# Kernel optimization log

Measured on AMD Instinct MI355X. Metric: run time of the kernel, lower is better.

## Reference

```python
import jax, jax.numpy as jnp
import numpy as np
from jax import lax

DIM = 128
N_CODEBOOKS = 8
CODEBOOK_SIZE = 2048
BATCH = 16
TOKENS = 2048


def setup_inputs() -> dict:
    key = jax.random.key(0)
    k1, k2 = jax.random.split(key)
    x = jax.random.normal(k1, (BATCH, DIM, TOKENS), dtype=jnp.float32)
    # matches nn.Parameter(torch.randn(K, D) / D**0.5) per stage, stacked
    codebooks = jax.random.normal(k2, (N_CODEBOOKS, CODEBOOK_SIZE, DIM),
                                  dtype=jnp.float32) / jnp.sqrt(jnp.float32(DIM))
    return {"x": x, "codebooks": codebooks}


def reference(x, codebooks):
    """Residual VQ forward.

    x: (B, D, T), codebooks: (n_cb, K, D)
    Returns (total_quantized (B,D,T), codes (B,n_cb,T) int32, commitment_loss scalar)
    """
    xt = jnp.transpose(x, (0, 2, 1))  # (B, T, D)

    def step(carry, cb):
        residual, total = carry  # (B,T,D) each; cb: (K,D)
        # squared euclidean distances: ||r||^2 - 2 r.c + ||c||^2 -> (B,T,K)
        dist = (jnp.sum(residual * residual, axis=-1, keepdims=True)
                - 2.0 * jnp.einsum('btd,kd->btk', residual, cb)
                + jnp.sum(cb * cb, axis=-1))
        idx = jnp.argmin(dist, axis=-1)          # (B, T)
        quantized = cb[idx]                       # gather -> (B, T, D)
        # straight-through combine
        q_st = residual + lax.stop_gradient(quantized - residual)
        total = total + q_st
        residual = residual - lax.stop_gradient(quantized)
        # F.mse_loss(residual.detach(), zeros) == mean(residual**2), detached
        loss = jnp.mean(lax.stop_gradient(residual) ** 2)
        return (residual, total), (idx.astype(jnp.int32), loss)

    init = (xt, jnp.zeros_like(xt))
    (_, total), (codes, losses) = lax.scan(step, init, codebooks)
    total_quantized = jnp.transpose(total, (0, 2, 1))   # (B, D, T)
    codes = jnp.transpose(codes, (1, 0, 2))             # (B, n_cb, T)
    commitment_loss = jnp.sum(losses)
    return total_quantized, codes, commitment_loss
```

## Files before the change

### kernel.cpp

```cpp
#include <hip/hip_runtime.h>

#define DIM 128
#define NCB 8
#define KSZ 2048
#define BATCH 16
#define TOK 2048
#define NTOK (BATCH * TOK)
#define NELEM (BATCH * DIM * TOK)
#define T_TILE 128
#define NTHR 512
#define CHUNK 32
#define NCHUNK 16
#define GCODES 512

typedef float f32x4 __attribute__((ext_vector_type(4)));
typedef _Float16 f16x8 __attribute__((ext_vector_type(8)));

__global__ void rvq_prep_f16(const float* __restrict__ cbs,
                             _Float16* __restrict__ chf) {
    int i = blockIdx.x * 256 + threadIdx.x;
    chf[i] = (_Float16)cbs[i];
}

__global__ void rvq_cnorm(const float* __restrict__ cbs,
                          float* __restrict__ cnorm,
                          float* __restrict__ loss_acc) {
    if (blockIdx.x == 0 && threadIdx.x == 0) *loss_acc = 0.0f;
    int k = blockIdx.x * 256 + threadIdx.x;
    const float4* row = (const float4*)(cbs + (size_t)k * DIM);
    float s = 0.0f;
#pragma unroll
    for (int i = 0; i < DIM / 4; ++i) {
        float4 v = row[i];
        s += v.x * v.x + v.y * v.y + v.z * v.z + v.w * v.w;
    }
    cnorm[k] = s;
}

__global__ __launch_bounds__(NTHR, 2) void rvq_fused(
        const float* __restrict__ x,
        const float* __restrict__ cbs,
        const _Float16* __restrict__ chf,
        const float* __restrict__ cng,
        float* __restrict__ out,
        float* __restrict__ codes,
        float* __restrict__ loss_acc) {
    __shared__ float res_lds[T_TILE][DIM + 4];
    __shared__ float cand[T_TILE * 132];
    __shared__ float cn_lds[KSZ];

    const int tid   = threadIdx.x;
    const int lane  = tid & 63;
    const int wv    = __builtin_amdgcn_readfirstlane(tid >> 6);
    const int col16 = lane & 15;
    const int quad  = lane >> 4;
    const int g     = wv >> 1;
    const int sub   = wv & 1;

    const int token0 = blockIdx.x * T_TILE;
    const int b      = token0 >> 11;
    const int t_in_b = token0 & (TOK - 1);

    {
        const float* xb = x + (size_t)b * DIM * TOK + t_in_b;
#pragma unroll
        for (int it = 0; it < 8; ++it) {
            int idx = it * NTHR + tid;
            int d  = idx >> 5;
            int t4 = (idx & 31) * 4;
            float4 v = *(const float4*)(xb + (size_t)d * TOK + t4);
            res_lds[t4 + 0][d] = v.x;
            res_lds[t4 + 1][d] = v.y;
            res_lds[t4 + 2][d] = v.z;
            res_lds[t4 + 3][d] = v.w;
        }
    }
    __syncthreads();

    float my_loss = 0.0f;
    const float INFV = __builtin_inff();

#define LOADB(dst)                                                             \
    {                                                                          \
        _Pragma("unroll")                                                      \
        for (int dc = 0; dc < 4; ++dc) {                                       \
            dst[dc]     = *(const f16x8*)(p0 + dc * 32);                       \
            dst[4 + dc] = *(const f16x8*)(p1 + dc * 32);                       \
        }                                                                      \
    }

#define COMPUTE(bX)                                                            \
    {                                                                          \
        _Pragma("unroll")                                                      \
        for (int mt = 0; mt < 4; ++mt) {                                       \
            acc[mt][0] = (f32x4){0.f, 0.f, 0.f, 0.f};                          \
            acc[mt][1] = (f32x4){0.f, 0.f, 0.f, 0.f};                          \
        }                                                                      \
        _Pragma("unroll")                                                      \
        for (int dc = 0; dc < 4; ++dc) {                                       \
            _Pragma("unroll")                                                  \
            for (int mt = 0; mt < 4; ++mt) {                                   \
                acc[mt][0] = __builtin_amdgcn_mfma_f32_16x16x32_f16(           \
                    ah[mt][dc], bX[dc], acc[mt][0], 0, 0, 0);                  \
                acc[mt][1] = __builtin_amdgcn_mfma_f32_16x16x32_f16(           \
                    ah[mt][dc], bX[4 + dc], acc[mt][1], 0, 0, 0);              \
            }                                                                  \
        }                                                                      \
    }

#define FOLD(cc)                                                               \
    {                                                                          \
        float cn0 = cn_lds[g * GCODES + (cc) * CHUNK + col16];                 \
        float cn1 = cn_lds[g * GCODES + (cc) * CHUNK + 16 + col16];            \
        unsigned em0 = ((unsigned)(cc) << 5) | (unsigned)col16;                \
        unsigned em1 = em0 | 16u;                                              \
        _Pragma("unroll")                                                      \
        for (int mt = 0; mt < 4; ++mt) {                                       \
            _Pragma("unroll")                                                  \
            for (int r = 0; r < 4; ++r) {                                      \
                int sl = mt * 4 + r;                                           \
                float p0s = fmaf(-2.0f, acc[mt][0][r], cn0);                   \
                float p1s = fmaf(-2.0f, acc[mt][1][r], cn1);                   \
                float q0 = __uint_as_float(                                    \
                    (__float_as_uint(p0s) & 0xFFFFFE00u) | em0);               \
                float q1 = __uint_as_float(                                    \
                    (__float_as_uint(p1s) & 0xFFFFFE00u) | em1);               \
                k2[sl] = fminf(k2[sl], fmaxf(k1[sl], q0));                     \
                k1[sl] = fminf(k1[sl], q0);                                    \
                k2[sl] = fminf(k2[sl], fmaxf(k1[sl], q1));                     \
                k1[sl] = fminf(k1[sl], q1);                                    \
            }                                                                  \
        }                                                                      \
    }

#pragma unroll 1
    for (int s = 0; s < NCB; ++s) {
        const _Float16* __restrict__ ch_s = chf + (size_t)s * KSZ * DIM;
        const float* __restrict__ cb_s = cbs + (size_t)s * KSZ * DIM;
        const float* __restrict__ cn_s = cng + (size_t)s * KSZ;

        const _Float16* p0 = ch_s + (size_t)(g * GCODES + col16) * DIM + quad * 8;
        const _Float16* p1 = p0 + 16 * DIM;
        f16x8 bA[8], bB[8];
        LOADB(bA);

        *(float4*)&cn_lds[tid * 4] = *(const float4*)(cn_s + tid * 4);

        f16x8 ah[4][4];
#pragma unroll
        for (int mt = 0; mt < 4; ++mt) {
#pragma unroll
            for (int dc = 0; dc < 4; ++dc) {
                int t  = sub * 64 + mt * 16 + col16;
                int d0 = dc * 32 + quad * 8;
                float4 u = *(const float4*)&res_lds[t][d0];
                float4 w = *(const float4*)&res_lds[t][d0 + 4];
                f16x8 hv;
                hv[0] = (_Float16)u.x; hv[1] = (_Float16)u.y;
                hv[2] = (_Float16)u.z; hv[3] = (_Float16)u.w;
                hv[4] = (_Float16)w.x; hv[5] = (_Float16)w.y;
                hv[6] = (_Float16)w.z; hv[7] = (_Float16)w.w;
                ah[mt][dc] = hv;
            }
        }

        float k1[16], k2[16];
#pragma unroll
        for (int sl = 0; sl < 16; ++sl) { k1[sl] = INFV; k2[sl] = INFV; }

        __syncthreads();

        f32x4 acc[4][2];
#pragma unroll 1
        for (int c = 0; c < NCHUNK; c += 2) {
            p0 += CHUNK * DIM; p1 += CHUNK * DIM;
            LOADB(bB);
            COMPUTE(bA);
            FOLD(c);
            if (c + 2 < NCHUNK) {
                p0 += CHUNK * DIM; p1 += CHUNK * DIM;
                LOADB(bA);
            }
            COMPUTE(bB);
            FOLD(c + 1);
        }

#pragma unroll
        for (int mt = 0; mt < 4; ++mt) {
#pragma unroll
            for (int r = 0; r < 4; ++r) {
                int t = sub * 64 + mt * 16 + quad * 4 + r;
                int sl = mt * 4 + r;
                float2 pr; pr.x = k1[sl]; pr.y = k2[sl];
                *(float2*)&cand[t * 132 + g * 32 + col16 * 2] = pr;
            }
        }
        __syncthreads();

        {
            const int t  = tid >> 2;
            const int gg = tid & 3;
            float bk0 = INFV, bk1 = INFV, bk2 = INFV, bk3 = INFV;
            const float* base = &cand[t * 132 + gg * 32];
#pragma unroll
            for (int j = 0; j < 8; ++j) {
                float4 v4 = *(const float4*)(base + j * 4);
                float vv[4] = {v4.x, v4.y, v4.z, v4.w};
#pragma unroll
                for (int e = 0; e < 4; ++e) {
                    float v = vv[e];
                    float M0 = fmaxf(bk0, v);  bk0 = fminf(bk0, v);
                    float M1 = fmaxf(bk1, M0); bk1 = fminf(bk1, M0);
                    float M2 = fmaxf(bk2, M1); bk2 = fminf(bk2, M1);
                    bk3 = fminf(bk3, M2);
                }
            }
            int cds[4];
            cds[0] = gg * GCODES + (int)(__float_as_uint(bk0) & 0x1FFu);
            cds[1] = gg * GCODES + (int)(__float_as_uint(bk1) & 0x1FFu);
            cds[2] = gg * GCODES + (int)(__float_as_uint(bk2) & 0x1FFu);
            cds[3] = gg * GCODES + (int)(__float_as_uint(bk3) & 0x1FFu);

            const float* q1p = cb_s + (size_t)cds[0] * DIM;
            const float* q2p = cb_s + (size_t)cds[1] * DIM;
            const float* q3p = cb_s + (size_t)cds[2] * DIM;
            const float* q4p = cb_s + (size_t)cds[3] * DIM;
            float n0 = 0, n1 = 0, n2 = 0, n3 = 0;
            float a[4][4];
#pragma unroll
            for (int jj = 0; jj < 4; ++jj)
#pragma unroll
                for (int e = 0; e < 4; ++e) a[jj][e] = 0.0f;
#pragma unroll 8
            for (int d4 = 0; d4 < DIM / 4; ++d4) {
                float4 r4 = *(const float4*)&res_lds[t][d4 * 4];
                n0 = fmaf(r4.x, r4.x, n0); n1 = fmaf(r4.y, r4.y, n1);
                n2 = fmaf(r4.z, r4.z, n2); n3 = fmaf(r4.w, r4.w, n3);
                float4 q0 = *(const float4*)(q1p + d4 * 4);
                a[0][0] = fmaf(r4.x, q0.x, a[0][0]);
                a[0][1] = fmaf(r4.y, q0.y, a[0][1]);
                a[0][2] = fmaf(r4.z, q0.z, a[0][2]);
                a[0][3] = fmaf(r4.w, q0.w, a[0][3]);
                float4 q1 = *(const float4*)(q2p + d4 * 4);
                a[1][0] = fmaf(r4.x, q1.x, a[1][0]);
                a[1][1] = fmaf(r4.y, q1.y, a[1][1]);
                a[1][2] = fmaf(r4.z, q1.z, a[1][2]);
                a[1][3] = fmaf(r4.w, q1.w, a[1][3]);
                float4 q2 = *(const float4*)(q3p + d4 * 4);
                a[2][0] = fmaf(r4.x, q2.x, a[2][0]);
                a[2][1] = fmaf(r4.y, q2.y, a[2][1]);
                a[2][2] = fmaf(r4.z, q2.z, a[2][2]);
                a[2][3] = fmaf(r4.w, q2.w, a[2][3]);
                float4 q3 = *(const float4*)(q4p + d4 * 4);
                a[3][0] = fmaf(r4.x, q3.x, a[3][0]);
                a[3][1] = fmaf(r4.y, q3.y, a[3][1]);
                a[3][2] = fmaf(r4.z, q3.z, a[3][2]);
                a[3][3] = fmaf(r4.w, q3.w, a[3][3]);
            }
            float rn = (n0 + n1) + (n2 + n3);
            float bd = INFV; int bc = 0x7FFFFFFF;
#pragma unroll
            for (int jj = 0; jj < 4; ++jj) {
                float dot = (a[jj][0] + a[jj][1]) + (a[jj][2] + a[jj][3]);
                float dist = fmaf(-2.0f, dot, rn) + cn_s[cds[jj]];
                if (dist < bd || (dist == bd && cds[jj] < bc)) {
                    bd = dist; bc = cds[jj];
                }
            }
#pragma unroll
            for (int mk = 1; mk <= 2; mk <<= 1) {
                float od = __shfl_xor(bd, mk, 64);
                int   oc = __shfl_xor(bc, mk, 64);
                if (od < bd || (od == bd && oc < bc)) { bd = od; bc = oc; }
            }
            if (gg == 0)
                codes[(size_t)b * (NCB * TOK) + (size_t)s * TOK + t_in_b + t] =
                    (float)bc;
            const float* qrow = cb_s + (size_t)bc * DIM;
            float lp = 0.0f;
#pragma unroll
            for (int d4 = 0; d4 < 8; ++d4) {
                int d = gg * 32 + d4 * 4;
                float4 r4 = *(const float4*)&res_lds[t][d];
                float4 q4 = *(const float4*)(qrow + d);
                float4 nr;
                nr.x = r4.x - q4.x; nr.y = r4.y - q4.y;
                nr.z = r4.z - q4.z; nr.w = r4.w - q4.w;
                *(float4*)&res_lds[t][d] = nr;
                lp += nr.x * nr.x + nr.y * nr.y + nr.z * nr.z + nr.w * nr.w;
            }
            my_loss += lp;
        }
        __syncthreads();
    }

    {
        const float* xb = x + (size_t)b * DIM * TOK + t_in_b;
        float* ob = out + (size_t)b * DIM * TOK + t_in_b;
#pragma unroll
        for (int it = 0; it < 8; ++it) {
            int idx = it * NTHR + tid;
            int d  = idx >> 5;
            int t4 = (idx & 31) * 4;
            float4 v = *(const float4*)(xb + (size_t)d * TOK + t4);
            float4 o;
            o.x = v.x - res_lds[t4 + 0][d];
            o.y = v.y - res_lds[t4 + 1][d];
            o.z = v.z - res_lds[t4 + 2][d];
            o.w = v.w - res_lds[t4 + 3][d];
            *(float4*)(ob + (size_t)d * TOK + t4) = o;
        }
    }

#pragma unroll
    for (int off = 32; off > 0; off >>= 1)
        my_loss += __shfl_down(my_loss, off, 64);
    if (lane == 0) atomicAdd(loss_acc, my_loss);
}

__global__ void rvq_loss_fin(const float* __restrict__ loss_acc,
                             float* __restrict__ loss_out) {
    *loss_out = *loss_acc * (1.0f / (float)NELEM);
}

extern "C" void kernel_launch(void* const* d_in, const int* in_sizes, int n_in,
                              void* d_out, int out_size, void* d_ws, size_t ws_size,
                              hipStream_t stream) {
    const float* x   = (const float*)d_in[0];
    const float* cbs = (const float*)d_in[1];

    float* out      = (float*)d_out;
    float* codes    = out + NELEM;
    float* loss_out = out + NELEM + (size_t)BATCH * NCB * TOK;

    float* wsf      = (float*)d_ws;
    float* loss_acc = wsf;
    _Float16* chf   = (_Float16*)(wsf + 256);
    float* cng      = (float*)(chf + (size_t)NCB * KSZ * DIM);

    hipLaunchKernelGGL(rvq_prep_f16, dim3((NCB * KSZ * DIM) / 256), dim3(256),
                       0, stream, cbs, chf);
    hipLaunchKernelGGL(rvq_cnorm, dim3((NCB * KSZ) / 256), dim3(256), 0, stream,
                       cbs, cng, loss_acc);
    hipLaunchKernelGGL(rvq_fused, dim3(NTOK / T_TILE), dim3(NTHR), 0, stream,
                       x, cbs, chf, cng, out, codes, loss_acc);
    hipLaunchKernelGGL(rvq_loss_fin, dim3(1), dim3(1), 0, stream,
                       loss_acc, loss_out);
}
```

Baseline: 606.3 us.

## Halve token tile and split candidate rescoring across lanes by dimension

Shrinks each block to 64 tokens and 256 threads, so each wave now covers all tokens of the tile for its codebook quarter. This roughly halves LDS per block, which should let two blocks share a CU and overlap each other's barrier and rescore phases. The exact rescore now pools the top-4 from all four groups into 16 candidates per token. Each of a token's four lanes scores every candidate over its own 32-dimension slice, reduces with cross-lane shuffles, and reads codebook norms from LDS. The cost is that every wave streams the full codebook quarter for only 64 tokens, doubling f16 codebook reads across the grid.

After: 571.5 us. -5.7%, faster.

```diff
diff --git a/kernel.cpp b/kernel.cpp
--- a/kernel.cpp
+++ b/kernel.cpp
@@ -7,8 +7,8 @@
 #define TOK 2048
 #define NTOK (BATCH * TOK)
 #define NELEM (BATCH * DIM * TOK)
-#define T_TILE 128
-#define NTHR 512
+#define T_TILE 64
+#define NTHR 256
 #define CHUNK 32
 #define NCHUNK 16
 #define GCODES 512
@@ -48,14 +48,13 @@
     __shared__ float res_lds[T_TILE][DIM + 4];
     __shared__ float cand[T_TILE * 132];
     __shared__ float cn_lds[KSZ];
+    __shared__ int   best16s[T_TILE][16];
 
     const int tid   = threadIdx.x;
     const int lane  = tid & 63;
-    const int wv    = __builtin_amdgcn_readfirstlane(tid >> 6);
+    const int g     = __builtin_amdgcn_readfirstlane(tid >> 6);
     const int col16 = lane & 15;
     const int quad  = lane >> 4;
-    const int g     = wv >> 1;
-    const int sub   = wv & 1;
 
     const int token0 = blockIdx.x * T_TILE;
     const int b      = token0 >> 11;
@@ -66,8 +65,8 @@
 #pragma unroll
         for (int it = 0; it < 8; ++it) {
             int idx = it * NTHR + tid;
-            int d  = idx >> 5;
-            int t4 = (idx & 31) * 4;
+            int d  = idx >> 4;
+            int t4 = (idx & 15) * 4;
             float4 v = *(const float4*)(xb + (size_t)d * TOK + t4);
             res_lds[t4 + 0][d] = v.x;
             res_lds[t4 + 1][d] = v.y;
@@ -144,14 +143,18 @@
         f16x8 bA[8], bB[8];
         LOADB(bA);
 
-        *(float4*)&cn_lds[tid * 4] = *(const float4*)(cn_s + tid * 4);
+#pragma unroll
+        for (int i = 0; i < 2; ++i) {
+            int idx = tid + i * NTHR;
+            *(float4*)&cn_lds[idx * 4] = *(const float4*)(cn_s + idx * 4);
+        }
 
         f16x8 ah[4][4];
 #pragma unroll
         for (int mt = 0; mt < 4; ++mt) {
 #pragma unroll
             for (int dc = 0; dc < 4; ++dc) {
-                int t  = sub * 64 + mt * 16 + col16;
+                int t  = mt * 16 + col16;
                 int d0 = dc * 32 + quad * 8;
                 float4 u = *(const float4*)&res_lds[t][d0];
                 float4 w = *(const float4*)&res_lds[t][d0 + 4];
@@ -189,7 +192,7 @@
         for (int mt = 0; mt < 4; ++mt) {
 #pragma unroll
             for (int r = 0; r < 4; ++r) {
-                int t = sub * 64 + mt * 16 + quad * 4 + r;
+                int t = mt * 16 + quad * 4 + r;
                 int sl = mt * 4 + r;
                 float2 pr; pr.x = k1[sl]; pr.y = k2[sl];
                 *(float2*)&cand[t * 132 + g * 32 + col16 * 2] = pr;
@@ -215,78 +218,68 @@
                     bk3 = fminf(bk3, M2);
                 }
             }
-            int cds[4];
-            cds[0] = gg * GCODES + (int)(__float_as_uint(bk0) & 0x1FFu);
-            cds[1] = gg * GCODES + (int)(__float_as_uint(bk1) & 0x1FFu);
-            cds[2] = gg * GCODES + (int)(__float_as_uint(bk2) & 0x1FFu);
-            cds[3] = gg * GCODES + (int)(__float_as_uint(bk3) & 0x1FFu);
-
-            const float* q1p = cb_s + (size_t)cds[0] * DIM;
-            const float* q2p = cb_s + (size_t)cds[1] * DIM;
-            const float* q3p = cb_s + (size_t)cds[2] * DIM;
-            const float* q4p = cb_s + (size_t)cds[3] * DIM;
+            best16s[t][gg * 4 + 0] = gg * GCODES + (int)(__float_as_uint(bk0) & 0x1FFu);
+            best16s[t][gg * 4 + 1] = gg * GCODES + (int)(__float_as_uint(bk1) & 0x1FFu);
+            best16s[t][gg * 4 + 2] = gg * GCODES + (int)(__float_as_uint(bk2) & 0x1FFu);
+            best16s[t][gg * 4 + 3] = gg * GCODES + (int)(__float_as_uint(bk3) & 0x1FFu);
+            int cds16[16];
+#pragma unroll
+            for (int jj = 0; jj < 16; ++jj) cds16[jj] = best16s[t][jj];
+
+            float4 rq[8];
+#pragma unroll
+            for (int d4 = 0; d4 < 8; ++d4)
+                rq[d4] = *(const float4*)&res_lds[t][gg * 32 + d4 * 4];
+
             float n0 = 0, n1 = 0, n2 = 0, n3 = 0;
-            float a[4][4];
-#pragma unroll
-            for (int jj = 0; jj < 4; ++jj)
-#pragma unroll
-                for (int e = 0; e < 4; ++e) a[jj][e] = 0.0f;
-#pragma unroll 8
-            for (int d4 = 0; d4 < DIM / 4; ++d4) {
-                float4 r4 = *(const float4*)&res_lds[t][d4 * 4];
-                n0 = fmaf(r4.x, r4.x, n0); n1 = fmaf(r4.y, r4.y, n1);
-                n2 = fmaf(r4.z, r4.z, n2); n3 = fmaf(r4.w, r4.w, n3);
-                float4 q0 = *(const float4*)(q1p + d4 * 4);
-                a[0][0] = fmaf(r4.x, q0.x, a[0][0]);
-                a[0][1] = fmaf(r4.y, q0.y, a[0][1]);
-                a[0][2] = fmaf(r4.z, q0.z, a[0][2]);
-                a[0][3] = fmaf(r4.w, q0.w, a[0][3]);
-                float4 q1 = *(const float4*)(q2p + d4 * 4);
-                a[1][0] = fmaf(r4.x, q1.x, a[1][0]);
-                a[1][1] = fmaf(r4.y, q1.y, a[1][1]);
-                a[1][2] = fmaf(r4.z, q1.z, a[1][2]);
-                a[1][3] = fmaf(r4.w, q1.w, a[1][3]);
-                float4 q2 = *(const float4*)(q3p + d4 * 4);
-                a[2][0] = fmaf(r4.x, q2.x, a[2][0]);
-                a[2][1] = fmaf(r4.y, q2.y, a[2][1]);
-                a[2][2] = fmaf(r4.z, q2.z, a[2][2]);
-                a[2][3] = fmaf(r4.w, q2.w, a[2][3]);
-                float4 q3 = *(const float4*)(q4p + d4 * 4);
-                a[3][0] = fmaf(r4.x, q3.x, a[3][0]);
-                a[3][1] = fmaf(r4.y, q3.y, a[3][1]);
-                a[3][2] = fmaf(r4.z, q3.z, a[3][2]);
-                a[3][3] = fmaf(r4.w, q3.w, a[3][3]);
+#pragma unroll
+            for (int d4 = 0; d4 < 8; ++d4) {
+                n0 = fmaf(rq[d4].x, rq[d4].x, n0);
+                n1 = fmaf(rq[d4].y, rq[d4].y, n1);
+                n2 = fmaf(rq[d4].z, rq[d4].z, n2);
+                n3 = fmaf(rq[d4].w, rq[d4].w, n3);
             }
             float rn = (n0 + n1) + (n2 + n3);
+            rn += __shfl_xor(rn, 1, 64);
+            rn += __shfl_xor(rn, 2, 64);
+
+            float dist16[16];
+#pragma unroll 4
+            for (int jj = 0; jj < 16; ++jj) {
+                const float* crow = cb_s + (size_t)cds16[jj] * DIM + gg * 32;
+                float a0 = 0, a1 = 0, a2 = 0, a3 = 0;
+#pragma unroll
+                for (int d4 = 0; d4 < 8; ++d4) {
+                    float4 q4 = *(const float4*)(crow + d4 * 4);
+                    a0 = fmaf(rq[d4].x, q4.x, a0);
+                    a1 = fmaf(rq[d4].y, q4.y, a1);
+                    a2 = fmaf(rq[d4].z, q4.z, a2);
+                    a3 = fmaf(rq[d4].w, q4.w, a3);
+                }
+                float pd = (a0 + a1) + (a2 + a3);
+                pd += __shfl_xor(pd, 1, 64);
+                pd += __shfl_xor(pd, 2, 64);
+                dist16[jj] = fmaf(-2.0f, pd, rn) + cn_lds[cds16[jj]];
+            }
             float bd = INFV; int bc = 0x7FFFFFFF;
 #pragma unroll
-            for (int jj = 0; jj < 4; ++jj) {
-                float dot = (a[jj][0] + a[jj][1]) + (a[jj][2] + a[jj][3]);
-                float dist = fmaf(-2.0f, dot, rn) + cn_s[cds[jj]];
-                if (dist < bd || (dist == bd && cds[jj] < bc)) {
-                    bd = dist; bc = cds[jj];
+            for (int jj = 0; jj < 16; ++jj) {
+                if (dist16[jj] < bd || (dist16[jj] == bd && cds16[jj] < bc)) {
+                    bd = dist16[jj]; bc = cds16[jj];
                 }
-            }
-#pragma unroll
-            for (int mk = 1; mk <= 2; mk <<= 1) {
-                float od = __shfl_xor(bd, mk, 64);
-                int   oc = __shfl_xor(bc, mk, 64);
-                if (od < bd || (od == bd && oc < bc)) { bd = od; bc = oc; }
             }
             if (gg == 0)
                 codes[(size_t)b * (NCB * TOK) + (size_t)s * TOK + t_in_b + t] =
                     (float)bc;
-            const float* qrow = cb_s + (size_t)bc * DIM;
+            const float* qrow = cb_s + (size_t)bc * DIM + gg * 32;
             float lp = 0.0f;
 #pragma unroll
             for (int d4 = 0; d4 < 8; ++d4) {
-                int d = gg * 32 + d4 * 4;
-                float4 r4 = *(const float4*)&res_lds[t][d];
-                float4 q4 = *(const float4*)(qrow + d);
+                float4 q4 = *(const float4*)(qrow + d4 * 4);
                 float4 nr;
-                nr.x = r4.x - q4.x; nr.y = r4.y - q4.y;
-                nr.z = r4.z - q4.z; nr.w = r4.w - q4.w;
-                *(float4*)&res_lds[t][d] = nr;
+                nr.x = rq[d4].x - q4.x; nr.y = rq[d4].y - q4.y;
+                nr.z = rq[d4].z - q4.z; nr.w = rq[d4].w - q4.w;
+                *(float4*)&res_lds[t][gg * 32 + d4 * 4] = nr;
                 lp += nr.x * nr.x + nr.y * nr.y + nr.z * nr.z + nr.w * nr.w;
             }
             my_loss += lp;
@@ -300,8 +293,8 @@
 #pragma unroll
         for (int it = 0; it < 8; ++it) {
             int idx = it * NTHR + tid;
-            int d  = idx >> 5;
-            int t4 = (idx & 31) * 4;
+            int d  = idx >> 4;
+            int t4 = (idx & 15) * 4;
             float4 v = *(const float4*)(xb + (size_t)d * TOK + t4);
             float4 o;
             o.x = v.x - res_lds[t4 + 0][d];
```
